# Optimization experiments

Measured on AMD Instinct MI355X. Metric: run time of the kernel, lower is better.

## Reference

```python
import jax, jax.numpy as jnp
import numpy as np

SPLINE_ORDER = 3
TOP_K = 2
NUM_EXPERTS = 8


def _gram_basis(x, beta_w):
    # x: (B, C, H, W) post-tanh. Returns (B, C*(S+1), H, W).
    P0 = jnp.ones_like(x)
    P1 = x
    ps = [P0, P1]
    for i in range(2, SPLINE_ORDER + 1):
        n, m = i - 1, i
        # beta(n, m) = (m+n)*(m-n)*n^2 / (m^2/(4n^2-1)) * beta_weights[n]
        beta = (m + n) * (m - n) * (n ** 2) * (4.0 * n ** 2 - 1.0) / (m ** 2) * beta_w[n]
        P2 = x * ps[-1] - beta * ps[-2]
        ps.append(P2)
    return jnp.concatenate(ps, axis=1)


def _expert(x, poly_w, beta_w):
    # tanh -> Gram polynomial basis -> SiLU -> conv2d (padding=1, stride=1)
    g = jax.nn.silu(_gram_basis(jnp.tanh(x), beta_w))
    return jax.lax.conv_general_dilated(
        g, poly_w[0], window_strides=(1, 1), padding=[(1, 1), (1, 1)],
        dimension_numbers=('NCHW', 'OIHW', 'NCHW'))


def _cv_squared(v):
    # torch.var is unbiased (ddof=1)
    return jnp.var(v, ddof=1) / (jnp.mean(v) ** 2 + 1e-10)


def reference(x, w_gate, poly_weights, beta_weights):
    B = x.shape[0]
    # gating input: global average pool -> (B, C)
    gate_x = jnp.mean(x, axis=(2, 3))
    probs = jax.nn.softmax(gate_x @ w_gate, axis=1)  # softmax BEFORE topk, as in source
    top_vals, top_idx = jax.lax.top_k(probs, TOP_K + 1)
    tk_vals = top_vals[:, :TOP_K]
    tk_idx = top_idx[:, :TOP_K]
    tk_gates = tk_vals / (jnp.sum(tk_vals, axis=1, keepdims=True) + 1e-6)
    gates = jnp.zeros_like(probs).at[jnp.arange(B)[:, None], tk_idx].set(tk_gates)
    importance = gates.sum(axis=0)
    load = jnp.sum(gates > 0, axis=0).astype(jnp.float32)  # eval-mode load
    loss = (_cv_squared(importance) + _cv_squared(load)) * 0.01
    # All experts share parameters (ModuleList([experts]*num_experts)), so
    # sum_e gates[b,e] * expert_e(x[b]) == gates.sum(1)[b] * expert(x[b]).
    y = _expert(x, poly_weights, beta_weights) * jnp.sum(gates, axis=1)[:, None, None, None]
    return y, loss


def setup_inputs() -> dict:
    key = jax.random.key(0)
    k1, k2, k3, k4 = jax.random.split(key, 4)
    x = jax.random.normal(k1, (16, 32, 192, 192), dtype=jnp.float32)
    w_gate = jax.random.normal(k2, (32, NUM_EXPERTS), dtype=jnp.float32) * 0.1
    poly_weights = jax.random.normal(k3, (1, 32, 32 * (SPLINE_ORDER + 1), 3, 3), dtype=jnp.float32) * 0.05
    beta_weights = jax.random.normal(k4, (SPLINE_ORDER + 1,), dtype=jnp.float32) * 0.01
    return {"x": x, "w_gate": w_gate, "poly_weights": poly_weights, "beta_weights": beta_weights}
```

## Files before the change

### kernel.cpp

```cpp
#include <hip/hip_runtime.h>

typedef unsigned short u16;
typedef unsigned int u32;
typedef __attribute__((ext_vector_type(8))) short bf16x8;
typedef __attribute__((ext_vector_type(4))) float f32x4;

static constexpr int B = 16, C = 32, H = 192, W = 192;
static constexpr int HW = H * W;
static constexpr int E = 8;
static constexpr int CO = 32;
static constexpr long long NTOT = (long long)B * C * HW;
static constexpr float SILU1 = 0.7310585786300049f;

static constexpr size_t GX_OFF = (size_t)NTOT * 2;
static constexpr size_t SK_OFF = GX_OFF + 512 * 4;
static constexpr size_t SS_OFF = SK_OFF + 288 * 4;
static constexpr size_t WF_OFF = SS_OFF + 128;

__device__ inline u16 f2b(float f) {
    u32 u = __float_as_uint(f);
    return (u16)((u + 0x7fffu + ((u >> 16) & 1u)) >> 16);
}
__device__ inline float silu(float z) { return z / (1.0f + __expf(-z)); }

__global__ __launch_bounds__(256) void stage1_prep(const float* __restrict__ x,
                                                   const float* __restrict__ pw,
                                                   u16* __restrict__ t_out,
                                                   float* __restrict__ gate_x,
                                                   float* __restrict__ Sk,
                                                   float* __restrict__ Ssum,
                                                   u16* __restrict__ wfrag) {
    const int blk = blockIdx.x, t = threadIdx.x;
    __shared__ float sred[9][32][8];
    if (blk < 512) {
        const float4* xp = (const float4*)(x + (size_t)blk * HW);
        ushort4* tp = (ushort4*)(t_out + (size_t)blk * HW);
        float s = 0.0f;
        for (int i = t; i < HW / 4; i += 256) {
            float4 v = xp[i];
            s += (v.x + v.y) + (v.z + v.w);
            ushort4 o;
            o.x = f2b(tanhf(v.x)); o.y = f2b(tanhf(v.y));
            o.z = f2b(tanhf(v.z)); o.w = f2b(tanhf(v.w));
            tp[i] = o;
        }
        #pragma unroll
        for (int off = 32; off > 0; off >>= 1) s += __shfl_down(s, off, 64);
        if ((t & 63) == 0) sred[0][0][t >> 6] = s;
        __syncthreads();
        if (t == 0)
            gate_x[blk] = (sred[0][0][0] + sred[0][0][1] + sred[0][0][2] + sred[0][0][3])
                          * (1.0f / HW);
        return;
    }
    if (blk < 620) {
        int j = (blk - 512) * 256 + t;
        int e = j & 7, lane = (j >> 3) & 63, rest = j >> 9;
        int half = rest & 1, pt = rest >> 1;
        int p = pt / 9, tap = pt - p * 9;
        int co = half * 16 + (lane & 15);
        int ci = 32 + p * 32 + (lane >> 4) * 8 + e;
        wfrag[j] = f2b(pw[(size_t)co * 1152 + ci * 9 + tap]);
        return;
    }
    {
        const int co = t & 31, sub = t >> 5;
        #pragma unroll
        for (int k = 0; k < 9; ++k) {
            float s = 0.0f;
            #pragma unroll
            for (int i = 0; i < 4; ++i)
                s += pw[(size_t)co * 1152 + (sub * 4 + i) * 9 + k];
            sred[k][co][sub] = s;
        }
        __syncthreads();
        __shared__ float sks[288];
        for (int j = t; j < 288; j += 256) {
            int k = j >> 5, c = j & 31;
            float s = 0.0f;
            #pragma unroll
            for (int u = 0; u < 8; ++u) s += sred[k][c][u];
            sks[j] = s; Sk[j] = s;
        }
        __syncthreads();
        if (t < 32) {
            float s = 0.0f;
            #pragma unroll
            for (int k = 0; k < 9; ++k) s += sks[k * 32 + t];
            Ssum[t] = s;
        }
    }
}

static constexpr int GSTR = 40;

__global__ __launch_bounds__(256) void conv_mfma(const u16* __restrict__ t_ws,
                                                 const u16* __restrict__ wfrag,
                                                 const float* __restrict__ beta_w,
                                                 const float* __restrict__ gate_x,
                                                 const float* __restrict__ wg,
                                                 const float* __restrict__ Sk,
                                                 const float* __restrict__ Ssum,
                                                 float* __restrict__ out) {
    __shared__ __align__(16) u16 gtile[324 * GSTR];
    __shared__ float lg[B][E];
    __shared__ float scl[B];

    const int b = blockIdx.z;
    const int gx0 = blockIdx.x << 4, gy0 = blockIdx.y << 4;
    const int tid = threadIdx.x;
    const int w = tid >> 6, lane = tid & 63, q = lane >> 4, ml = lane & 15;
    const float beta2 = 2.25f * beta_w[1];
    const float beta23 = beta2 + (300.0f / 9.0f) * beta_w[2];

    const int p0 = tid;
    int extra = -1;
    if ((tid & 3) == 0) extra = tid >> 2;
    else if ((tid & 63) == 1) extra = 64 + (tid >> 6);
    const int p1 = (extra >= 0) ? 256 + extra : -1;

    u32 pk0[16], pk1[16];
    bool v0, v1 = false;
    {
        int py = p0 / 18, px = p0 - py * 18;
        int gy = gy0 + py - 1, gx = gx0 + px - 1;
        v0 = (unsigned)gy < (unsigned)H && (unsigned)gx < (unsigned)W;
        #pragma unroll
        for (int cc = 0; cc < 16; ++cc) pk0[cc] = 0u;
        if (v0) {
            const u16* tp = t_ws + (size_t)b * C * HW + gy * W + gx;
            #pragma unroll
            for (int cc = 0; cc < 16; ++cc) {
                u32 lo = tp[(size_t)(2 * cc) * HW];
                u32 hi = tp[(size_t)(2 * cc + 1) * HW];
                pk0[cc] = lo | (hi << 16);
            }
        }
        #pragma unroll
        for (int cc = 0; cc < 16; ++cc) pk1[cc] = 0u;
        if (p1 >= 0) {
            int py1 = p1 / 18, px1 = p1 - py1 * 18;
            int gy1 = gy0 + py1 - 1, gx1 = gx0 + px1 - 1;
            v1 = (unsigned)gy1 < (unsigned)H && (unsigned)gx1 < (unsigned)W;
            if (v1) {
                const u16* tp = t_ws + (size_t)b * C * HW + gy1 * W + gx1;
                #pragma unroll
                for (int cc = 0; cc < 16; ++cc) {
                    u32 lo = tp[(size_t)(2 * cc) * HW];
                    u32 hi = tp[(size_t)(2 * cc + 1) * HW];
                    pk1[cc] = lo | (hi << 16);
                }
            }
        }
    }

    if (tid < 128) {
        int gb = tid >> 3, ge = tid & 7;
        float s = 0.0f;
        #pragma unroll
        for (int c = 0; c < 32; ++c) s += gate_x[gb * 32 + c] * wg[c * 8 + ge];
        lg[gb][ge] = s;
    }
    __syncthreads();
    if (tid < 16) {
        float p[E];
        float m = lg[tid][0];
        #pragma unroll
        for (int e = 1; e < E; ++e) m = fmaxf(m, lg[tid][e]);
        float sum = 0.0f;
        #pragma unroll
        for (int e = 0; e < E; ++e) { p[e] = __expf(lg[tid][e] - m); sum += p[e]; }
        float inv = 1.0f / sum;
        #pragma unroll
        for (int e = 0; e < E; ++e) p[e] *= inv;
        int i0 = 0; float v0g = p[0];
        #pragma unroll
        for (int e = 1; e < E; ++e) if (p[e] > v0g) { v0g = p[e]; i0 = e; }
        int i1 = -1; float v1g = -1.0f;
        #pragma unroll
        for (int e = 0; e < E; ++e) { if (e == i0) continue; if (p[e] > v1g) { v1g = p[e]; i1 = e; } }
        const float denom = v0g + v1g + 1e-6f;
        const float g0 = v0g / denom, g1 = v1g / denom;
        #pragma unroll
        for (int e = 0; e < E; ++e) lg[tid][e] = 0.0f;
        lg[tid][i0] = g0; lg[tid][i1] = g1;
        scl[tid] = g0 + g1;
    }
    __syncthreads();
    if (blockIdx.x == 0 && blockIdx.y == 0 && b == 0 && tid == 0) {
        float imp[E], ld[E];
        #pragma unroll
        for (int e = 0; e < E; ++e) { imp[e] = 0.0f; ld[e] = 0.0f; }
        for (int bb = 0; bb < B; ++bb)
            #pragma unroll
            for (int e = 0; e < E; ++e) {
                float g = lg[bb][e];
                imp[e] += g;
                if (g > 0.0f) ld[e] += 1.0f;
            }
        float mi = 0.0f, mld = 0.0f;
        #pragma unroll
        for (int e = 0; e < E; ++e) { mi += imp[e]; mld += ld[e]; }
        mi *= (1.0f / E); mld *= (1.0f / E);
        float vi = 0.0f, vl = 0.0f;
        #pragma unroll
        for (int e = 0; e < E; ++e) {
            float di = imp[e] - mi, dl = ld[e] - mld;
            vi += di * di; vl += dl * dl;
        }
        vi *= (1.0f / (E - 1)); vl *= (1.0f / (E - 1));
        out[NTOT] = (vi / (mi * mi + 1e-10f) + vl / (mld * mld + 1e-10f)) * 0.01f;
    }

    f32x4 acc[4][2];
    #pragma unroll
    for (int a = 0; a < 4; ++a) {
        acc[a][0] = (f32x4){0.0f, 0.0f, 0.0f, 0.0f};
        acc[a][1] = (f32x4){0.0f, 0.0f, 0.0f, 0.0f};
    }

    #pragma unroll
    for (int p = 0; p < 3; ++p) {
        if (p) __syncthreads();
        #pragma unroll
        for (int slot = 0; slot < 2; ++slot) {
            const int pix = slot ? p1 : p0;
            if (slot && p1 < 0) continue;
            const bool vv = slot ? v1 : v0;
            const u32* pk = slot ? pk1 : pk0;
            u32 r[16];
            if (vv) {
                #pragma unroll
                for (int cc = 0; cc < 16; ++cc) {
                    float tl = __uint_as_float(pk[cc] << 16);
                    float th = __uint_as_float(pk[cc] & 0xffff0000u);
                    float ul, uh;
                    if (p == 0) { ul = tl; uh = th; }
                    else if (p == 1) { ul = fmaf(tl, tl, -beta2); uh = fmaf(th, th, -beta2); }
                    else { ul = tl * fmaf(tl, tl, -beta23); uh = th * fmaf(th, th, -beta23); }
                    u32 gl = __float_as_uint(silu(ul)) + 0x8000u;
                    u32 gh = __float_as_uint(silu(uh)) + 0x8000u;
                    r[cc] = (gl >> 16) | (gh & 0xffff0000u);
                }
            } else {
                #pragma unroll
                for (int cc = 0; cc < 16; ++cc) r[cc] = 0u;
            }
            uint4* dst = (uint4*)&gtile[pix * GSTR];
            dst[0] = *(const uint4*)&r[0];
            dst[1] = *(const uint4*)&r[4];
            dst[2] = *(const uint4*)&r[8];
            dst[3] = *(const uint4*)&r[12];
        }
        __syncthreads();
        const u16* wf = wfrag + (size_t)p * 9216;
        #pragma unroll
        for (int dx = 0; dx < 3; ++dx) {
            bf16x8 bf[3][2];
            #pragma unroll
            for (int dyi = 0; dyi < 3; ++dyi) {
                const int tap = dyi * 3 + dx;
                bf[dyi][0] = *(const bf16x8*)(wf + ((size_t)(tap * 2 + 0) * 64 + lane) * 8);
                bf[dyi][1] = *(const bf16x8*)(wf + ((size_t)(tap * 2 + 1) * 64 + lane) * 8);
            }
            #pragma unroll
            for (int rl = 0; rl < 6; ++rl) {
                const bf16x8 af = *(const bf16x8*)
                    &gtile[(((w << 2) + rl) * 18 + ml + dx) * GSTR + (q << 3)];
                #pragma unroll
                for (int dyi = 0; dyi < 3; ++dyi) {
                    const int a = rl - dyi;
                    if (a >= 0 && a < 4) {
                        acc[a][0] = __builtin_amdgcn_mfma_f32_16x16x32_bf16(af, bf[dyi][0], acc[a][0], 0, 0, 0);
                        acc[a][1] = __builtin_amdgcn_mfma_f32_16x16x32_bf16(af, bf[dyi][1], acc[a][1], 0, 0, 0);
                    }
                }
            }
        }
    }

    const float sc = scl[b];
    const bool interior = (blockIdx.x > 0) && (blockIdx.x < 11) &&
                          (blockIdx.y > 0) && (blockIdx.y < 11);
    #pragma unroll
    for (int half = 0; half < 2; ++half) {
        const int co = half * 16 + ml;
        const float bfull = SILU1 * Ssum[co];
        #pragma unroll
        for (int a = 0; a < 4; ++a) {
            const int y = gy0 + (w << 2) + a;
            float ov[4];
            #pragma unroll
            for (int r = 0; r < 4; ++r) {
                float bias = bfull;
                if (!interior) {
                    const int xg = gx0 + (q << 2) + r;
                    bias = 0.0f;
                    #pragma unroll
                    for (int k = 0; k < 9; ++k) {
                        int yy = y + k / 3 - 1, xx = xg + k % 3 - 1;
                        if ((unsigned)yy < (unsigned)H && (unsigned)xx < (unsigned)W)
                            bias += Sk[k * 32 + co];
                    }
                    bias *= SILU1;
                }
                ov[r] = (acc[a][half][r] + bias) * sc;
            }
            *(float4*)&out[((size_t)(b * CO + co) * H + y) * W + gx0 + (q << 2)] = *(float4*)ov;
        }
    }
}

extern "C" void kernel_launch(void* const* d_in, const int* in_sizes, int n_in,
                              void* d_out, int out_size, void* d_ws, size_t ws_size,
                              hipStream_t stream) {
    const float* x  = (const float*)d_in[0];
    const float* wg = (const float*)d_in[1];
    const float* pw = (const float*)d_in[2];
    const float* bw = (const float*)d_in[3];
    float* out = (float*)d_out;
    char* ws = (char*)d_ws;
    u16*   t_ws   = (u16*)ws;
    float* gate_x = (float*)(ws + GX_OFF);
    float* Sk     = (float*)(ws + SK_OFF);
    float* Ssum   = (float*)(ws + SS_OFF);
    u16*   wfrag  = (u16*)(ws + WF_OFF);

    stage1_prep<<<dim3(621), 256, 0, stream>>>(x, pw, t_ws, gate_x, Sk, Ssum, wfrag);
    conv_mfma<<<dim3(12, 12, B), 256, 0, stream>>>(t_ws, wfrag, bw, gate_x, wg, Sk, Ssum, out);
}
```

Measured before the change: 290.7 us.

## Store tanh activations channel-interleaved and move gating into a separate kernel

The bf16 tanh intermediate is now written pixel-major with all 32 channels contiguous, so each conv block can load a halo pixel with four 16-byte vector loads instead of 32 strided 2-byte loads. The prep kernel is split into 1536 row-band blocks that write partial channel sums, and a new single-block gate kernel reduces them and does softmax, top-k and the loss once. This removes the gating recomputation from every conv block. It also swaps tanhf for an exp/rcp approximation and adds one extra kernel launch.

```diff
diff --git a/kernel.cpp b/kernel.cpp
--- a/kernel.cpp
+++ b/kernel.cpp
@@ -9,52 +9,73 @@
 static constexpr int HW = H * W;
 static constexpr int E = 8;
 static constexpr int CO = 32;
+static constexpr int NB = 96;
 static constexpr long long NTOT = (long long)B * C * HW;
 static constexpr float SILU1 = 0.7310585786300049f;
 
-static constexpr size_t GX_OFF = (size_t)NTOT * 2;
-static constexpr size_t SK_OFF = GX_OFF + 512 * 4;
-static constexpr size_t SS_OFF = SK_OFF + 288 * 4;
-static constexpr size_t WF_OFF = SS_OFF + 128;
+static constexpr size_t GP_OFF  = (size_t)NTOT * 2;
+static constexpr size_t SCL_OFF = GP_OFF + (size_t)B * C * NB * 4;
+static constexpr size_t SK_OFF  = SCL_OFF + 128;
+static constexpr size_t SS_OFF  = SK_OFF + 288 * 4;
+static constexpr size_t WF_OFF  = SS_OFF + 128;
 
 __device__ inline u16 f2b(float f) {
     u32 u = __float_as_uint(f);
     return (u16)((u + 0x7fffu + ((u >> 16) & 1u)) >> 16);
 }
 __device__ inline float silu(float z) { return z / (1.0f + __expf(-z)); }
+__device__ inline float tanh_fast(float z) {
+    float e = __expf(2.0f * z);
+    return 1.0f - 2.0f * __builtin_amdgcn_rcpf(e + 1.0f);
+}
 
 __global__ __launch_bounds__(256) void stage1_prep(const float* __restrict__ x,
                                                    const float* __restrict__ pw,
                                                    u16* __restrict__ t_out,
-                                                   float* __restrict__ gate_x,
+                                                   float* __restrict__ gpart,
                                                    float* __restrict__ Sk,
                                                    float* __restrict__ Ssum,
                                                    u16* __restrict__ wfrag) {
-    const int blk = blockIdx.x, t = threadIdx.x;
+    __shared__ float sg[2][4][16];
     __shared__ float sred[9][32][8];
-    if (blk < 512) {
-        const float4* xp = (const float4*)(x + (size_t)blk * HW);
-        ushort4* tp = (ushort4*)(t_out + (size_t)blk * HW);
-        float s = 0.0f;
-        for (int i = t; i < HW / 4; i += 256) {
-            float4 v = xp[i];
-            s += (v.x + v.y) + (v.z + v.w);
-            ushort4 o;
-            o.x = f2b(tanhf(v.x)); o.y = f2b(tanhf(v.y));
-            o.z = f2b(tanhf(v.z)); o.w = f2b(tanhf(v.w));
-            tp[i] = o;
-        }
-        #pragma unroll
-        for (int off = 32; off > 0; off >>= 1) s += __shfl_down(s, off, 64);
-        if ((t & 63) == 0) sred[0][0][t >> 6] = s;
+    __shared__ float sks[288];
+    const int blk = blockIdx.x, tid = threadIdx.x;
+    if (blk < B * NB) {
+        const int b = blk / NB, band = blk - (blk / NB) * NB;
+        const int cp = tid & 15, part = tid >> 4;
+        const size_t pbase = (size_t)b * HW + (size_t)(band * 2) * W;
+        const float4* xa = (const float4*)(x + (size_t)(b * C + 2 * cp) * HW
+                                             + (size_t)(band * 2) * W);
+        const float4* xb = (const float4*)(x + (size_t)(b * C + 2 * cp + 1) * HW
+                                             + (size_t)(band * 2) * W);
+        u32* tw = (u32*)t_out;
+        float s0 = 0.0f, s1 = 0.0f;
+        #pragma unroll
+        for (int k = 0; k < 6; ++k) {
+            const int j = k * 16 + part;
+            float4 a = xa[j], c = xb[j];
+            s0 += (a.x + a.y) + (a.z + a.w);
+            s1 += (c.x + c.y) + (c.z + c.w);
+            u32 r0 = (u32)f2b(tanh_fast(a.x)) | ((u32)f2b(tanh_fast(c.x)) << 16);
+            u32 r1 = (u32)f2b(tanh_fast(a.y)) | ((u32)f2b(tanh_fast(c.y)) << 16);
+            u32 r2 = (u32)f2b(tanh_fast(a.z)) | ((u32)f2b(tanh_fast(c.z)) << 16);
+            u32 r3 = (u32)f2b(tanh_fast(a.w)) | ((u32)f2b(tanh_fast(c.w)) << 16);
+            u32* dst = tw + (pbase + (size_t)j * 4) * 16 + cp;
+            dst[0] = r0; dst[16] = r1; dst[32] = r2; dst[48] = r3;
+        }
+        s0 += __shfl_down(s0, 32); s0 += __shfl_down(s0, 16);
+        s1 += __shfl_down(s1, 32); s1 += __shfl_down(s1, 16);
+        if ((part & 3) == 0) { sg[0][tid >> 6][cp] = s0; sg[1][tid >> 6][cp] = s1; }
         __syncthreads();
-        if (t == 0)
-            gate_x[blk] = (sred[0][0][0] + sred[0][0][1] + sred[0][0][2] + sred[0][0][3])
-                          * (1.0f / HW);
+        if (tid < 32) {
+            const int cpp = tid >> 1, o = tid & 1;
+            gpart[(size_t)(b * C + tid) * NB + band] =
+                (sg[o][0][cpp] + sg[o][1][cpp]) + (sg[o][2][cpp] + sg[o][3][cpp]);
+        }
         return;
     }
-    if (blk < 620) {
-        int j = (blk - 512) * 256 + t;
+    if (blk < B * NB + 108) {
+        int j = (blk - B * NB) * 256 + tid;
         int e = j & 7, lane = (j >> 3) & 63, rest = j >> 9;
         int half = rest & 1, pt = rest >> 1;
         int p = pt / 9, tap = pt - p * 9;
@@ -64,7 +85,7 @@
         return;
     }
     {
-        const int co = t & 31, sub = t >> 5;
+        const int co = tid & 31, sub = tid >> 5;
         #pragma unroll
         for (int k = 0; k < 9; ++k) {
             float s = 0.0f;
@@ -74,8 +95,7 @@
             sred[k][co][sub] = s;
         }
         __syncthreads();
-        __shared__ float sks[288];
-        for (int j = t; j < 288; j += 256) {
+        for (int j = tid; j < 288; j += 256) {
             int k = j >> 5, c = j & 31;
             float s = 0.0f;
             #pragma unroll
@@ -83,12 +103,86 @@
             sks[j] = s; Sk[j] = s;
         }
         __syncthreads();
-        if (t < 32) {
+        if (tid < 32) {
             float s = 0.0f;
             #pragma unroll
-            for (int k = 0; k < 9; ++k) s += sks[k * 32 + t];
-            Ssum[t] = s;
-        }
+            for (int k = 0; k < 9; ++k) s += sks[k * 32 + tid];
+            Ssum[tid] = s;
+        }
+    }
+}
+
+__global__ __launch_bounds__(512) void gate_k(const float* __restrict__ gpart,
+                                              const float* __restrict__ wg,
+                                              float* __restrict__ scl,
+                                              float* __restrict__ out) {
+    __shared__ float gx[B][C];
+    __shared__ float lg[B][E];
+    __shared__ float gt[B][E];
+    const int tid = threadIdx.x;
+    {
+        const float4* gp = (const float4*)(gpart + (size_t)tid * NB);
+        float s = 0.0f;
+        #pragma unroll
+        for (int k = 0; k < NB / 4; ++k) { float4 v = gp[k]; s += (v.x + v.y) + (v.z + v.w); }
+        gx[tid >> 5][tid & 31] = s * (1.0f / HW);
+    }
+    __syncthreads();
+    if (tid < B * E) {
+        const int gb = tid >> 3, ge = tid & 7;
+        float s = 0.0f;
+        #pragma unroll
+        for (int c = 0; c < C; ++c) s += gx[gb][c] * wg[c * E + ge];
+        lg[gb][ge] = s;
+    }
+    __syncthreads();
+    if (tid < B) {
+        float p[E];
+        float m = lg[tid][0];
+        #pragma unroll
+        for (int e = 1; e < E; ++e) m = fmaxf(m, lg[tid][e]);
+        float sum = 0.0f;
+        #pragma unroll
+        for (int e = 0; e < E; ++e) { p[e] = __expf(lg[tid][e] - m); sum += p[e]; }
+        float inv = 1.0f / sum;
+        #pragma unroll
+        for (int e = 0; e < E; ++e) p[e] *= inv;
+        int i0 = 0; float v0g = p[0];
+        #pragma unroll
+        for (int e = 1; e < E; ++e) if (p[e] > v0g) { v0g = p[e]; i0 = e; }
+        int i1 = -1; float v1g = -1.0f;
+        #pragma unroll
+        for (int e = 0; e < E; ++e) { if (e == i0) continue; if (p[e] > v1g) { v1g = p[e]; i1 = e; } }
+        const float denom = v0g + v1g + 1e-6f;
+        #pragma unroll
+        for (int e = 0; e < E; ++e) gt[tid][e] = 0.0f;
+        gt[tid][i0] = v0g / denom; gt[tid][i1] = v1g / denom;
+        scl[tid] = gt[tid][i0] + gt[tid][i1];
+    }
+    __syncthreads();
+    if (tid == 0) {
+        float imp[E], ld[E];
+        #pragma unroll
+        for (int e = 0; e < E; ++e) { imp[e] = 0.0f; ld[e] = 0.0f; }
+        for (int bb = 0; bb < B; ++bb)
+            #pragma unroll
+            for (int e = 0; e < E; ++e) {
+                float g = gt[bb][e];
+                imp[e] += g;
+                if (g > 0.0f) ld[e] += 1.0f;
+            }
+        float mi = 0.0f, mld = 0.0f;
+        #pragma unroll
+        for (int e = 0; e < E; ++e) { mi += imp[e]; mld += ld[e]; }
+        mi *= (1.0f / E); mld *= (1.0f / E);
+        float vi = 0.0f, vl = 0.0f;
+        #pragma unroll
+        for (int e = 0; e < E; ++e) {
+            float di = imp[e] - mi, dl = ld[e] - mld;
+            vi += di * di; vl += dl * dl;
+        }
+        vi *= (1.0f / (E - 1)); vl *= (1.0f / (E - 1));
+        out[NTOT] = (vi / (mi * mi + 1e-10f) + vl / (mld * mld + 1e-10f)) * 0.01f;
     }
 }
 
@@ -97,14 +191,11 @@
 __global__ __launch_bounds__(256) void conv_mfma(const u16* __restrict__ t_ws,
                                                  const u16* __restrict__ wfrag,
                                                  const float* __restrict__ beta_w,
-                                                 const float* __restrict__ gate_x,
-                                                 const float* __restrict__ wg,
+                                                 const float* __restrict__ scl_ws,
                                                  const float* __restrict__ Sk,
                                                  const float* __restrict__ Ssum,
                                                  float* __restrict__ out) {
     __shared__ __align__(16) u16 gtile[324 * GSTR];
-    __shared__ float lg[B][E];
-    __shared__ float scl[B];
 
     const int b = blockIdx.z;
     const int gx0 = blockIdx.x << 4, gy0 = blockIdx.y << 4;
@@ -125,92 +216,35 @@
         int py = p0 / 18, px = p0 - py * 18;
         int gy = gy0 + py - 1, gx = gx0 + px - 1;
         v0 = (unsigned)gy < (unsigned)H && (unsigned)gx < (unsigned)W;
-        #pragma unroll
-        for (int cc = 0; cc < 16; ++cc) pk0[cc] = 0u;
         if (v0) {
-            const u16* tp = t_ws + (size_t)b * C * HW + gy * W + gx;
-            #pragma unroll
-            for (int cc = 0; cc < 16; ++cc) {
-                u32 lo = tp[(size_t)(2 * cc) * HW];
-                u32 hi = tp[(size_t)(2 * cc + 1) * HW];
-                pk0[cc] = lo | (hi << 16);
-            }
-        }
-        #pragma unroll
-        for (int cc = 0; cc < 16; ++cc) pk1[cc] = 0u;
+            const uint4* tp = (const uint4*)(t_ws + (((size_t)b * HW + (size_t)gy * W + gx) << 5));
+            *(uint4*)&pk0[0]  = tp[0];
+            *(uint4*)&pk0[4]  = tp[1];
+            *(uint4*)&pk0[8]  = tp[2];
+            *(uint4*)&pk0[12] = tp[3];
+        } else {
+            #pragma unroll
+            for (int cc = 0; cc < 16; ++cc) pk0[cc] = 0u;
+        }
         if (p1 >= 0) {
             int py1 = p1 / 18, px1 = p1 - py1 * 18;
             int gy1 = gy0 + py1 - 1, gx1 = gx0 + px1 - 1;
             v1 = (unsigned)gy1 < (unsigned)H && (unsigned)gx1 < (unsigned)W;
             if (v1) {
-                const u16* tp = t_ws + (size_t)b * C * HW + gy1 * W + gx1;
-                #pragma unroll
-                for (int cc = 0; cc < 16; ++cc) {
-                    u32 lo = tp[(size_t)(2 * cc) * HW];
-                    u32 hi = tp[(size_t)(2 * cc + 1) * HW];
-                    pk1[cc] = lo | (hi << 16);
-                }
-            }
-        }
-    }
-
-    if (tid < 128) {
-        int gb = tid >> 3, ge = tid & 7;
-        float s = 0.0f;
-        #pragma unroll
-        for (int c = 0; c < 32; ++c) s += gate_x[gb * 32 + c] * wg[c * 8 + ge];
-        lg[gb][ge] = s;
-    }
-    __syncthreads();
-    if (tid < 16) {
-        float p[E];
-        float m = lg[tid][0];
-        #pragma unroll
-        for (int e = 1; e < E; ++e) m = fmaxf(m, lg[tid][e]);
-        float sum = 0.0f;
-        #pragma unroll
-        for (int e = 0; e < E; ++e) { p[e] = __expf(lg[tid][e] - m); sum += p[e]; }
-        float inv = 1.0f / sum;
-        #pragma unroll
-        for (int e = 0; e < E; ++e) p[e] *= inv;
-        int i0 = 0; float v0g = p[0];
-        #pragma unroll
-        for (int e = 1; e < E; ++e) if (p[e] > v0g) { v0g = p[e]; i0 = e; }
-        int i1 = -1; float v1g = -1.0f;
-        #pragma unroll
-        for (int e = 0; e < E; ++e) { if (e == i0) continue; if (p[e] > v1g) { v1g = p[e]; i1 = e; } }
-        const float denom = v0g + v1g + 1e-6f;
-        const float g0 = v0g / denom, g1 = v1g / denom;
-        #pragma unroll
-        for (int e = 0; e < E; ++e) lg[tid][e] = 0.0f;
-        lg[tid][i0] = g0; lg[tid][i1] = g1;
-        scl[tid] = g0 + g1;
-    }
-    __syncthreads();
-    if (blockIdx.x == 0 && blockIdx.y == 0 && b == 0 && tid == 0) {
-        float imp[E], ld[E];
-        #pragma unroll
-        for (int e = 0; e < E; ++e) { imp[e] = 0.0f; ld[e] = 0.0f; }
-        for (int bb = 0; bb < B; ++bb)
-            #pragma unroll
-            for (int e = 0; e < E; ++e) {
-                float g = lg[bb][e];
-                imp[e] += g;
-                if (g > 0.0f) ld[e] += 1.0f;
-            }
-        float mi = 0.0f, mld = 0.0f;
-        #pragma unroll
-        for (int e = 0; e < E; ++e) { mi += imp[e]; mld += ld[e]; }
-        mi *= (1.0f / E); mld *= (1.0f / E);
-        float vi = 0.0f, vl = 0.0f;
-        #pragma unroll
-        for (int e = 0; e < E; ++e) {
-            float di = imp[e] - mi, dl = ld[e] - mld;
-            vi += di * di; vl += dl * dl;
-        }
-        vi *= (1.0f / (E - 1)); vl *= (1.0f / (E - 1));
-        out[NTOT] = (vi / (mi * mi + 1e-10f) + vl / (mld * mld + 1e-10f)) * 0.01f;
-    }
+                const uint4* tp = (const uint4*)(t_ws + (((size_t)b * HW + (size_t)gy1 * W + gx1) << 5));
+                *(uint4*)&pk1[0]  = tp[0];
+                *(uint4*)&pk1[4]  = tp[1];
+                *(uint4*)&pk1[8]  = tp[2];
+                *(uint4*)&pk1[12] = tp[3];
+            }
+        }
+        if (!v1) {
+            #pragma unroll
+            for (int cc = 0; cc < 16; ++cc) pk1[cc] = 0u;
+        }
+    }
+
+    const float sc = scl_ws[b];
 
     f32x4 acc[4][2];
     #pragma unroll
@@ -279,7 +313,6 @@
         }
     }
 
-    const float sc = scl[b];
     const bool interior = (blockIdx.x > 0) && (blockIdx.x < 11) &&
                           (blockIdx.y > 0) && (blockIdx.y < 11);
     #pragma unroll
@@ -320,12 +353,14 @@
     const float* bw = (const float*)d_in[3];
     float* out = (float*)d_out;
     char* ws = (char*)d_ws;
-    u16*   t_ws   = (u16*)ws;
-    float* gate_x = (float*)(ws + GX_OFF);
-    float* Sk     = (float*)(ws + SK_OFF);
-    float* Ssum   = (float*)(ws + SS_OFF);
-    u16*   wfrag  = (u16*)(ws + WF_OFF);
-
-    stage1_prep<<<dim3(621), 256, 0, stream>>>(x, pw, t_ws, gate_x, Sk, Ssum, wfrag);
-    conv_mfma<<<dim3(12, 12, B), 256, 0, stream>>>(t_ws, wfrag, bw, gate_x, wg, Sk, Ssum, out);
-}
+    u16*   t_ws  = (u16*)ws;
+    float* gpart = (float*)(ws + GP_OFF);
+    float* scl   = (float*)(ws + SCL_OFF);
+    float* Sk    = (float*)(ws + SK_OFF);
+    float* Ssum  = (float*)(ws + SS_OFF);
+    u16*   wfrag = (u16*)(ws + WF_OFF);
+
+    stage1_prep<<<dim3(B * NB + 109), 256, 0, stream>>>(x, pw, t_ws, gpart, Sk, Ssum, wfrag);
+    gate_k<<<dim3(1), 512, 0, stream>>>(gpart, wg, scl, out);
+    conv_mfma<<<dim3(12, 12, B), 256, 0, stream>>>(t_ws, wfrag, bw, scl, Sk, Ssum, out);
+}
```

Measured after the change: 267.2 us. -8.1%, faster.
